# Kernel optimization log

Measured on AMD Instinct MI355X. Metric: run time of the kernel, lower is better.

## Reference

```python
import jax, jax.numpy as jnp
import numpy as np

N_HEAD = 16
N_KV = 4
HEAD_DIM = 128
EPS = 1e-6


def setup_inputs() -> dict:
    key = jax.random.key(0)
    k1, k2, k3 = jax.random.split(key, 3)
    d_model = N_HEAD * HEAD_DIM
    qkv_out = (N_HEAD + 2 * N_KV) * HEAD_DIM
    B, T = 2, 2048
    x = jax.random.normal(k1, (B, T, d_model), dtype=jnp.float32)
    W_qkv = jax.random.normal(k2, (d_model, qkv_out), dtype=jnp.float32) * (d_model ** -0.5)
    W_proj = jax.random.normal(k3, (d_model, d_model), dtype=jnp.float32) * (d_model ** -0.5)
    q_scale = jnp.ones((HEAD_DIM,), dtype=jnp.float32)
    k_scale = jnp.ones((HEAD_DIM,), dtype=jnp.float32)
    return {"x": x, "W_qkv": W_qkv, "W_proj": W_proj, "q_scale": q_scale, "k_scale": k_scale}


def _rms_norm(t):
    return t * jax.lax.rsqrt(jnp.mean(t * t, axis=-1, keepdims=True) + EPS)


def reference(x, W_qkv, W_proj, q_scale, k_scale):
    B, T, C = x.shape
    qkv = x @ W_qkv  # [B, T, (H+2*KV)*D]
    q, k, v = jnp.split(qkv, [N_HEAD * HEAD_DIM, (N_HEAD + N_KV) * HEAD_DIM], axis=-1)
    q = q.reshape(B, T, N_HEAD, HEAD_DIM).transpose(0, 2, 1, 3)  # [B,H,T,D]
    k = k.reshape(B, T, N_KV, HEAD_DIM).transpose(0, 2, 1, 3)    # [B,KV,T,D]
    v = v.reshape(B, T, N_KV, HEAD_DIM).transpose(0, 2, 1, 3)
    # QK RMS-norm with learned per-dim scales
    q = _rms_norm(q) * q_scale
    k = _rms_norm(k) * k_scale
    # GQA: repeat kv heads to match query heads
    rep = N_HEAD // N_KV
    k = jnp.repeat(k, rep, axis=1)
    v = jnp.repeat(v, rep, axis=1)
    # causal SDPA
    scale = 1.0 / jnp.sqrt(jnp.float32(HEAD_DIM))
    scores = jnp.einsum('bhqd,bhkd->bhqk', q, k) * scale
    causal = jnp.tril(jnp.ones((T, T), dtype=bool))
    scores = jnp.where(causal, scores, jnp.finfo(scores.dtype).min)
    attn = jax.nn.softmax(scores, axis=-1)
    y = jnp.einsum('bhqk,bhkd->bhqd', attn, v)  # [B,H,T,D]
    y = y.transpose(0, 2, 1, 3).reshape(B, T, C)
    return y @ W_proj
```

## Files before the change

kernel.cpp:

```cpp
#include <hip/hip_runtime.h>

typedef __bf16 bf16;
typedef __bf16 bf16x8 __attribute__((ext_vector_type(8)));
typedef __bf16 bf16x4 __attribute__((ext_vector_type(4)));
typedef float f32x4 __attribute__((ext_vector_type(4)));
typedef float f32x16 __attribute__((ext_vector_type(16)));
typedef unsigned u32x4 __attribute__((ext_vector_type(4)));

#define EXP2F(x) __builtin_amdgcn_exp2f(x)

#define LOAD_LDS16(gp, lp)                                                     \
  __builtin_amdgcn_global_load_lds(                                            \
      (const __attribute__((address_space(1))) void*)(gp),                     \
      (__attribute__((address_space(3))) void*)(lp), 16, 0, 0)

__global__ __launch_bounds__(256) void k_cvt_x(const float* __restrict__ in,
                                               bf16* __restrict__ out, int n4) {
  int i = blockIdx.x * 256 + threadIdx.x;
  if (i < n4) {
    float4 v = ((const float4*)in)[i];
    bf16x4 o = {(bf16)v.x, (bf16)v.y, (bf16)v.z, (bf16)v.w};
    ((bf16x4*)out)[i] = o;
  }
}

__global__ __launch_bounds__(256) void k_transpose(const float* __restrict__ in,
                                                   bf16* __restrict__ out,
                                                   int R, int C) {
  __shared__ bf16 t[64 * 65];
  int tid = threadIdx.x;
  int c0 = blockIdx.x * 64, r0 = blockIdx.y * 64;
#pragma unroll
  for (int i = 0; i < 16; ++i) {
    int f = i * 256 + tid;
    int rl = f >> 6, cl = f & 63;
    t[rl * 65 + cl] = (bf16)in[(size_t)(r0 + rl) * C + c0 + cl];
  }
  __syncthreads();
#pragma unroll
  for (int i = 0; i < 16; ++i) {
    int f = i * 256 + tid;
    int cl = f >> 6, rl = f & 63;
    out[(size_t)(c0 + cl) * R + r0 + rl] = t[rl * 65 + cl];
  }
}

template <typename OutT, int BM>
__global__ __launch_bounds__(512, 2) void k_gemm256(const bf16* __restrict__ A,
                                                    const bf16* __restrict__ Bt,
                                                    OutT* __restrict__ C,
                                                    int M, int N, int K) {
  constexpr int ASZ = 4 * BM * 8;
  constexpr int MREP = BM / 32;
  __shared__ alignas(16) bf16 As[2][2][ASZ];
  __shared__ alignas(16) bf16 Bs[2][2][4 * 256 * 8];
  int tid = threadIdx.x;
  int wid = tid >> 6, lane = tid & 63;
  int g = lane >> 4, lr = lane & 15;
  int wrow = (wid >> 2) * (BM / 2), wcol = (wid & 3) * 64;
  int gx = gridDim.x;
  int flat = blockIdx.y * gx + blockIdx.x;
  int cpx = (gx * gridDim.y) >> 3;
  int f2 = (flat & 7) * cpx + (flat >> 3);
  int row0 = (f2 % gx) * BM, col0 = (f2 / gx) * 256;
  int NT = K >> 6;
  f32x4 acc[MREP][4] = {};

  auto stageA = [&](int buf, int kh, int kt) {
#pragma unroll
    for (int pass = 0; pass < BM / 128; ++pass) {
      int slot = pass * 512 + tid;
      int kseg, row;
      if constexpr (BM == 256) { kseg = slot >> 8; row = slot & 255; }
      else { kseg = slot >> 7; row = slot & 127; }
      LOAD_LDS16(A + (size_t)(row0 + row) * K + kt * 64 + kh * 32 + kseg * 8,
                 &As[buf][kh][slot * 8]);
    }
  };
  auto stageB = [&](int buf, int kh, int kt) {
#pragma unroll
    for (int pass = 0; pass < 2; ++pass) {
      int slot = pass * 512 + tid;
      int kseg = slot >> 8, row = slot & 255;
      LOAD_LDS16(Bt + (size_t)(col0 + row) * K + kt * 64 + kh * 32 + kseg * 8,
                 &Bs[buf][kh][slot * 8]);
    }
  };
  auto dsA = [&](int buf, int s, int mq, bf16x8* af) {
#pragma unroll
    for (int i = 0; i < 4; ++i)
      af[i] = *(const bf16x8*)&As[buf][s]
                  [(g * BM + wrow + (mq * 4 + i) * 16 + lr) * 8];
  };
  auto dsB = [&](int buf, int s, bf16x8* bfr) {
#pragma unroll
    for (int i = 0; i < 4; ++i)
      bfr[i] = *(const bf16x8*)&Bs[buf][s][((g << 8) + wcol + i * 16 + lr) * 8];
  };
  auto mfma16 = [&](int mq, bf16x8* af, bf16x8* bfr) {
    __builtin_amdgcn_s_setprio(1);
#pragma unroll
    for (int i = 0; i < 4; ++i)
#pragma unroll
      for (int n = 0; n < 4; ++n)
        acc[mq * 4 + i][n] = __builtin_amdgcn_mfma_f32_16x16x32_bf16(
            af[i], bfr[n], acc[mq * 4 + i][n], 0, 0, 0);
    __builtin_amdgcn_s_setprio(0);
  };

  stageA(0, 0, 0);
  stageB(0, 0, 0);
  stageA(0, 1, 0);
  stageB(0, 1, 0);
  if constexpr (BM == 256)
    asm volatile("s_waitcnt vmcnt(4)" ::: "memory");
  else
    asm volatile("s_waitcnt vmcnt(3)" ::: "memory");
  __builtin_amdgcn_s_barrier();

  for (int T = 0; T < NT; ++T) {
    int buf = T & 1, nbuf = buf ^ 1;
    bool more = (T + 1 < NT);
    bf16x8 af[4], bfr[4];
    if constexpr (BM == 256) {
      dsA(buf, 0, 0, af);
      dsB(buf, 0, bfr);
      if (more) stageA(nbuf, 0, T + 1);
      __builtin_amdgcn_s_barrier();
      mfma16(0, af, bfr);
      __builtin_amdgcn_s_barrier();
      dsA(buf, 0, 1, af);
      if (more) {
        stageB(nbuf, 0, T + 1);
        asm volatile("s_waitcnt vmcnt(4)" ::: "memory");
      } else {
        asm volatile("s_waitcnt vmcnt(0)" ::: "memory");
      }
      __builtin_amdgcn_s_barrier();
      mfma16(1, af, bfr);
      __builtin_amdgcn_s_barrier();
      dsA(buf, 1, 0, af);
      dsB(buf, 1, bfr);
      if (more) stageA(nbuf, 1, T + 1);
      __builtin_amdgcn_s_barrier();
      mfma16(0, af, bfr);
      __builtin_amdgcn_s_barrier();
      dsA(buf, 1, 1, af);
      if (more) {
        stageB(nbuf, 1, T + 1);
        asm volatile("s_waitcnt vmcnt(4)" ::: "memory");
      }
      __builtin_amdgcn_s_barrier();
      mfma16(1, af, bfr);
      __builtin_amdgcn_s_barrier();
    } else {
      dsA(buf, 0, 0, af);
      dsB(buf, 0, bfr);
      if (more) {
        stageA(nbuf, 0, T + 1);
        stageB(nbuf, 0, T + 1);
        asm volatile("s_waitcnt vmcnt(3)" ::: "memory");
      } else {
        asm volatile("s_waitcnt vmcnt(0)" ::: "memory");
      }
      __builtin_amdgcn_s_barrier();
      mfma16(0, af, bfr);
      __builtin_amdgcn_s_barrier();
      dsA(buf, 1, 0, af);
      dsB(buf, 1, bfr);
      if (more) {
        stageA(nbuf, 1, T + 1);
        stageB(nbuf, 1, T + 1);
        asm volatile("s_waitcnt vmcnt(3)" ::: "memory");
      }
      __builtin_amdgcn_s_barrier();
      mfma16(0, af, bfr);
      __builtin_amdgcn_s_barrier();
    }
  }

#pragma unroll
  for (int mi = 0; mi < MREP; ++mi)
#pragma unroll
    for (int ni = 0; ni < 4; ++ni) {
      int rb = row0 + wrow + mi * 16 + g * 4;
      int cc = col0 + wcol + ni * 16 + lr;
#pragma unroll
      for (int r = 0; r < 4; ++r) {
        float v = acc[mi][ni][r];
        C[(size_t)(rb + r) * N + cc] = (OutT)v;
      }
    }
}

__global__ __launch_bounds__(256) void k_qknorm(bf16* __restrict__ qkv,
                                                const float* __restrict__ qs,
                                                const float* __restrict__ ks) {
  int tok = blockIdx.x;
  int wid = threadIdx.x >> 6, lane = threadIdx.x & 63;
  int d = lane * 2;
  bf16* rowp = qkv + (size_t)tok * 3072;
#pragma unroll
  for (int i = 0; i < 5; ++i) {
    int cb = (i < 4) ? (wid + i * 4) * 128 : 2048 + wid * 128;
    float v0 = (float)rowp[cb + d], v1 = (float)rowp[cb + d + 1];
    float ss = v0 * v0 + v1 * v1;
#pragma unroll
    for (int off = 1; off < 64; off <<= 1) ss += __shfl_xor(ss, off);
    float r = rsqrtf(ss * (1.0f / 128.0f) + 1e-6f);
    float s0, s1, extra;
    if (i < 4) {
      s0 = qs[d]; s1 = qs[d + 1];
      extra = 0.08838834764831845f * 1.4426950408889634f;
    } else {
      s0 = ks[d]; s1 = ks[d + 1]; extra = 1.0f;
    }
    rowp[cb + d] = (bf16)(v0 * r * s0 * extra);
    rowp[cb + d + 1] = (bf16)(v1 * r * s1 * extra);
  }
}

__global__ __launch_bounds__(256) void k_vt(const bf16* __restrict__ qkv,
                                            bf16* __restrict__ Vt) {
  __shared__ bf16 t[64 * 65];
  int tid = threadIdx.x;
  int t0 = blockIdx.x * 64, d0 = blockIdx.y * 64;
  int bh = blockIdx.z;
  int b = bh >> 2, kvh = bh & 3;
  const bf16* src = qkv + (size_t)(b * 2048) * 3072 + 2560 + kvh * 128;
  bf16* dst = Vt + (size_t)bh * 128 * 2048;
#pragma unroll
  for (int i = 0; i < 16; ++i) {
    int f = i * 256 + tid;
    int tl = f >> 6, dl = f & 63;
    t[tl * 65 + dl] = src[(size_t)(t0 + tl) * 3072 + d0 + dl];
  }
  __syncthreads();
#pragma unroll
  for (int i = 0; i < 16; ++i) {
    int f = i * 256 + tid;
    int dl = f >> 6, tl = f & 63;
    dst[(size_t)(d0 + dl) * 2048 + t0 + tl] = t[tl * 65 + dl];
  }
}

__device__ inline unsigned pack2bf(float a, float b) {
  union { bf16 h[2]; unsigned u; } x;
  x.h[0] = (bf16)a;
  x.h[1] = (bf16)b;
  return x.u;
}

__global__ __launch_bounds__(256, 2) void k_attn(const bf16* __restrict__ qkv,
                                                 const bf16* __restrict__ Vt,
                                                 bf16* __restrict__ y) {
  int flat = blockIdx.x;
  int xcd = flat & 7, iw = flat >> 3;
  int h = xcd + 8 * (iw & 1);
  int rem = iw >> 1;
  int b = rem >> 4;
  int qt = 15 - (rem & 15);
  int kvh = h >> 2;
  int tid = threadIdx.x;
  int wid = tid >> 6, lane = tid & 63;
  int qc = lane & 31, hi = lane >> 5;
  __shared__ alignas(16) bf16 Ks[2][16 * 64 * 8];
  __shared__ alignas(16) bf16 Vs[2][128 * 64];
  const bf16* Qb = qkv + (size_t)(b * 2048) * 3072 + h * 128;
  const bf16* Kb = qkv + (size_t)(b * 2048) * 3072 + 2048 + kvh * 128;
  const bf16* Vb = Vt + (size_t)(b * 4 + kvh) * 128 * 2048;
  int qw0 = qt * 128 + wid * 32;
  int qg = qw0 + qc;
  bf16x8 qf[8];
#pragma unroll
  for (int s = 0; s < 8; ++s)
    qf[s] = *(const bf16x8*)&Qb[(size_t)qg * 3072 + s * 16 + hi * 8];
  f32x16 acc[4] = {};
  float mrun = -1e30f, lrun = 0.f;

  auto STAGE = [&](int buf, int kt2) {
    int s0 = kt2 * 64;
#pragma unroll
    for (int i = 0; i < 4; ++i) {
      int slot = i * 256 + tid;
      int ch = slot >> 6, row = slot & 63;
      LOAD_LDS16(Kb + (size_t)(s0 + row) * 3072 + ch * 8, &Ks[buf][slot * 8]);
    }
#pragma unroll
    for (int i = 0; i < 4; ++i) {
      int slot = i * 256 + tid;
      int d = slot >> 3, c = slot & 7;
      LOAD_LDS16(Vb + (size_t)d * 2048 + s0 + ((c ^ (d & 7)) * 8),
                 &Vs[buf][slot * 8]);
    }
  };

  STAGE(0, 0);
  int cur = 0;
  int ktmax = 2 * qt + 1;
  for (int kt = 0; kt <= ktmax; ++kt) {
    int s0 = kt * 64;
    if (kt < ktmax) {
      STAGE(cur ^ 1, kt + 1);
      asm volatile("s_waitcnt vmcnt(8)" ::: "memory");
    } else {
      asm volatile("s_waitcnt vmcnt(0)" ::: "memory");
    }
    __builtin_amdgcn_s_barrier();
    __builtin_amdgcn_sched_barrier(0);
    if (s0 <= qw0 + 31) {
      f32x16 sc[2] = {};
#pragma unroll
      for (int s = 0; s < 8; ++s)
#pragma unroll
        for (int n = 0; n < 2; ++n) {
          bf16x8 kf =
              *(const bf16x8*)&Ks[cur][(((2 * s + hi) << 6) + n * 32 + qc) * 8];
          sc[n] =
              __builtin_amdgcn_mfma_f32_32x32x16_bf16(kf, qf[s], sc[n], 0, 0, 0);
        }
      if (s0 + 63 > qw0) {
#pragma unroll
        for (int n = 0; n < 2; ++n)
#pragma unroll
          for (int r = 0; r < 16; ++r) {
            int kg = s0 + n * 32 + (r & 3) + 8 * (r >> 2) + 4 * hi;
            if (kg > qg) sc[n][r] = -1e30f;
          }
      }
      float pm = -1e30f;
#pragma unroll
      for (int n = 0; n < 2; ++n)
#pragma unroll
        for (int r = 0; r < 16; ++r) pm = fmaxf(pm, sc[n][r]);
      pm = fmaxf(pm, __shfl_xor(pm, 32));
      if (__any(pm > mrun + 11.0f)) {
        float mnew = fmaxf(mrun, pm);
        float scl = EXP2F(mrun - mnew);
        mrun = mnew;
        lrun *= scl;
        float sv[16];
#pragma unroll
        for (int r = 0; r < 16; ++r)
          sv[r] = __shfl(scl, (r & 3) + 8 * (r >> 2) + 4 * hi);
#pragma unroll
        for (int dt = 0; dt < 4; ++dt)
#pragma unroll
          for (int r = 0; r < 16; ++r) acc[dt][r] *= sv[r];
      }
      float rs = 0.f;
#pragma unroll
      for (int n = 0; n < 2; ++n) {
        unsigned pk[8];
#pragma unroll
        for (int mm = 0; mm < 8; ++mm) {
          float e0 = EXP2F(sc[n][2 * mm] - mrun);
          float e1 = EXP2F(sc[n][2 * mm + 1] - mrun);
          rs += e0 + e1;
          pk[mm] = pack2bf(e0, e1);
        }
#pragma unroll
        for (int l2 = 0; l2 < 2; ++l2) {
          unsigned a0 = pk[4 * l2 + 0], b0 = pk[4 * l2 + 2];
          unsigned a1 = pk[4 * l2 + 1], b1 = pk[4 * l2 + 3];
          asm volatile("v_permlane32_swap_b32 %0, %1" : "+v"(a0), "+v"(b0));
          asm volatile("v_permlane32_swap_b32 %0, %1" : "+v"(a1), "+v"(b1));
          u32x4 w = {a0, a1, b0, b1};
          bf16x8 pf = __builtin_bit_cast(bf16x8, w);
          int ksg = 2 * n + l2;
#pragma unroll
          for (int dt = 0; dt < 4; ++dt) {
            int drow = dt * 32 + qc;
            bf16x8 vf = *(const bf16x8*)&Vs[cur][(drow * 8 +
                                                  ((2 * ksg + hi) ^ (qc & 7))) *
                                                 8];
            acc[dt] =
                __builtin_amdgcn_mfma_f32_32x32x16_bf16(pf, vf, acc[dt], 0, 0, 0);
          }
        }
      }
      rs += __shfl_xor(rs, 32);
      lrun += rs;
    }
    __builtin_amdgcn_s_barrier();
    cur ^= 1;
  }
  float rlv = 1.0f / lrun;
  float rcl[16];
#pragma unroll
  for (int r = 0; r < 16; ++r)
    rcl[r] = __shfl(rlv, (r & 3) + 8 * (r >> 2) + 4 * hi);
#pragma unroll
  for (int dt = 0; dt < 4; ++dt)
#pragma unroll
    for (int r = 0; r < 16; ++r) {
      int row = qw0 + (r & 3) + 8 * (r >> 2) + 4 * hi;
      float v = acc[dt][r] * rcl[r];
      y[(size_t)(b * 2048 + row) * 2048 + h * 128 + dt * 32 + qc] = (bf16)v;
    }
}

extern "C" void kernel_launch(void* const* d_in, const int* in_sizes, int n_in,
                              void* d_out, int out_size, void* d_ws,
                              size_t ws_size, hipStream_t stream) {
  const float* x = (const float*)d_in[0];
  const float* Wqkv = (const float*)d_in[1];
  const float* Wproj = (const float*)d_in[2];
  const float* qs = (const float*)d_in[3];
  const float* ks = (const float*)d_in[4];
  float* out = (float*)d_out;
  char* ws = (char*)d_ws;

  bf16* xb = (bf16*)(ws);
  bf16* Wqkvt = (bf16*)(ws + (size_t)(16u << 20));
  bf16* Wprojt = (bf16*)(ws + (size_t)(28u << 20));
  bf16* qkv = (bf16*)(ws + (size_t)(36u << 20));
  bf16* Vt = Wqkvt;
  bf16* y = xb;

  k_cvt_x<<<8192, 256, 0, stream>>>(x, xb, 8388608 / 4);
  k_transpose<<<dim3(3072 / 64, 2048 / 64), 256, 0, stream>>>(Wqkv, Wqkvt, 2048, 3072);
  k_transpose<<<dim3(2048 / 64, 2048 / 64), 256, 0, stream>>>(Wproj, Wprojt, 2048, 2048);
  k_gemm256<bf16, 256><<<dim3(16, 12), 512, 0, stream>>>(xb, Wqkvt, qkv, 4096, 3072, 2048);
  k_qknorm<<<4096, 256, 0, stream>>>(qkv, qs, ks);
  k_vt<<<dim3(32, 2, 8), 256, 0, stream>>>(qkv, Vt);
  k_attn<<<dim3(512, 1, 1), 256, 0, stream>>>(qkv, Vt, y);
  k_gemm256<float, 128><<<dim3(32, 8), 512, 0, stream>>>(y, Wprojt, out, 4096, 2048, 2048);
}
```

Baseline: 259.4 us.

## Use 128x128 GEMM for QKV projection and pre-tile V for contiguous attention loads

Adds a 128x128-tile, 256-thread GEMM kernel and uses it for the QKV projection, giving 768 workgroups in place of 192 for better CU occupancy. The V transpose now writes V in a chunked [tile][kchunk][d][8] layout so attention staging can load each 64-key tile as one contiguous block. The XOR-swizzled LDS reads for V are replaced with direct indexing, and a sched_barrier is added before the loop-end barrier. The risk is that the unswizzled V LDS reads cause bank conflicts, and the simpler GEMM pipeline waits on vmcnt(0) every iteration.

Result: slower. 290.5 us (+12.0%).

```diff
diff --git a/kernel.cpp b/kernel.cpp
--- a/kernel.cpp
+++ b/kernel.cpp
@@ -43,6 +43,85 @@
     int cl = f >> 6, rl = f & 63;
     out[(size_t)(c0 + cl) * R + r0 + rl] = t[rl * 65 + cl];
   }
+}
+
+template <typename OutT>
+__global__ __launch_bounds__(256, 3) void k_gemm128(const bf16* __restrict__ A,
+                                                    const bf16* __restrict__ Bt,
+                                                    OutT* __restrict__ C,
+                                                    int M, int N, int K) {
+  __shared__ alignas(16) bf16 As[2][4 * 128 * 8];
+  __shared__ alignas(16) bf16 Bs[2][4 * 128 * 8];
+  int tid = threadIdx.x;
+  int wid = tid >> 6, lane = tid & 63;
+  int g = lane >> 4, lr = lane & 15;
+  int wrow = (wid >> 1) * 64, wcol = (wid & 1) * 64;
+  int gx = gridDim.x;
+  int flat = blockIdx.y * gx + blockIdx.x;
+  int cpx = (gx * gridDim.y) >> 3;
+  int f2 = (flat & 7) * cpx + (flat >> 3);
+  int row0 = (f2 % gx) * 128, col0 = (f2 / gx) * 128;
+  int NT = K >> 5;
+  f32x4 acc[4][4] = {};
+
+  auto stageA = [&](int buf, int kt) {
+#pragma unroll
+    for (int pass = 0; pass < 2; ++pass) {
+      int slot = pass * 256 + tid;
+      int kseg = slot >> 7, row = slot & 127;
+      LOAD_LDS16(A + (size_t)(row0 + row) * K + kt * 32 + kseg * 8,
+                 &As[buf][slot * 8]);
+    }
+  };
+  auto stageB = [&](int buf, int kt) {
+#pragma unroll
+    for (int pass = 0; pass < 2; ++pass) {
+      int slot = pass * 256 + tid;
+      int kseg = slot >> 7, row = slot & 127;
+      LOAD_LDS16(Bt + (size_t)(col0 + row) * K + kt * 32 + kseg * 8,
+                 &Bs[buf][slot * 8]);
+    }
+  };
+
+  stageA(0, 0);
+  stageB(0, 0);
+  asm volatile("s_waitcnt vmcnt(0)" ::: "memory");
+  __builtin_amdgcn_s_barrier();
+
+  for (int T = 0; T < NT; ++T) {
+    int buf = T & 1;
+    if (T + 1 < NT) {
+      stageA(buf ^ 1, T + 1);
+      stageB(buf ^ 1, T + 1);
+    }
+    bf16x8 af[4], bfr[4];
+#pragma unroll
+    for (int i = 0; i < 4; ++i)
+      af[i] = *(const bf16x8*)&As[buf][((g << 7) + wrow + i * 16 + lr) * 8];
+#pragma unroll
+    for (int i = 0; i < 4; ++i)
+      bfr[i] = *(const bf16x8*)&Bs[buf][((g << 7) + wcol + i * 16 + lr) * 8];
+    __builtin_amdgcn_s_setprio(1);
+#pragma unroll
+    for (int i = 0; i < 4; ++i)
+#pragma unroll
+      for (int n = 0; n < 4; ++n)
+        acc[i][n] = __builtin_amdgcn_mfma_f32_16x16x32_bf16(af[i], bfr[n],
+                                                            acc[i][n], 0, 0, 0);
+    __builtin_amdgcn_s_setprio(0);
+    asm volatile("s_waitcnt vmcnt(0)" ::: "memory");
+    __builtin_amdgcn_s_barrier();
+  }
+
+#pragma unroll
+  for (int mi = 0; mi < 4; ++mi)
+#pragma unroll
+    for (int ni = 0; ni < 4; ++ni) {
+      int rb = row0 + wrow + mi * 16 + g * 4;
+      int cc = col0 + wcol + ni * 16 + lr;
+#pragma unroll
+      for (int r = 0; r < 4; ++r) C[(size_t)(rb + r) * N + cc] = (OutT)acc[mi][ni][r];
+    }
 }
 
 template <typename OutT, int BM>
@@ -186,10 +265,7 @@
       int rb = row0 + wrow + mi * 16 + g * 4;
       int cc = col0 + wcol + ni * 16 + lr;
 #pragma unroll
-      for (int r = 0; r < 4; ++r) {
-        float v = acc[mi][ni][r];
-        C[(size_t)(rb + r) * N + cc] = (OutT)v;
-      }
+      for (int r = 0; r < 4; ++r) C[(size_t)(rb + r) * N + cc] = (OutT)acc[mi][ni][r];
     }
 }
 
@@ -228,7 +304,7 @@
   int bh = blockIdx.z;
   int b = bh >> 2, kvh = bh & 3;
   const bf16* src = qkv + (size_t)(b * 2048) * 3072 + 2560 + kvh * 128;
-  bf16* dst = Vt + (size_t)bh * 128 * 2048;
+  bf16* dst = Vt + (size_t)bh * 262144 + (size_t)(t0 >> 6) * 8192;
 #pragma unroll
   for (int i = 0; i < 16; ++i) {
     int f = i * 256 + tid;
@@ -237,10 +313,13 @@
   }
   __syncthreads();
 #pragma unroll
-  for (int i = 0; i < 16; ++i) {
-    int f = i * 256 + tid;
-    int dl = f >> 6, tl = f & 63;
-    dst[(size_t)(d0 + dl) * 2048 + t0 + tl] = t[tl * 65 + dl];
+  for (int i = 0; i < 2; ++i) {
+    int v = i * 256 + tid;
+    int c = v >> 6, dv = v & 63;
+    bf16x8 o;
+#pragma unroll
+    for (int j = 0; j < 8; ++j) o[j] = t[(c * 8 + j) * 65 + dv];
+    *(bf16x8*)&dst[(size_t)c * 1024 + (size_t)(d0 + dv) * 8] = o;
   }
 }
 
@@ -265,10 +344,10 @@
   int wid = tid >> 6, lane = tid & 63;
   int qc = lane & 31, hi = lane >> 5;
   __shared__ alignas(16) bf16 Ks[2][16 * 64 * 8];
-  __shared__ alignas(16) bf16 Vs[2][128 * 64];
+  __shared__ alignas(16) bf16 Vs[2][8 * 128 * 8];
   const bf16* Qb = qkv + (size_t)(b * 2048) * 3072 + h * 128;
   const bf16* Kb = qkv + (size_t)(b * 2048) * 3072 + 2048 + kvh * 128;
-  const bf16* Vb = Vt + (size_t)(b * 4 + kvh) * 128 * 2048;
+  const bf16* Vb = Vt + (size_t)(b * 4 + kvh) * 262144;
   int qw0 = qt * 128 + wid * 32;
   int qg = qw0 + qc;
   bf16x8 qf[8];
@@ -289,9 +368,7 @@
 #pragma unroll
     for (int i = 0; i < 4; ++i) {
       int slot = i * 256 + tid;
-      int d = slot >> 3, c = slot & 7;
-      LOAD_LDS16(Vb + (size_t)d * 2048 + s0 + ((c ^ (d & 7)) * 8),
-                 &Vs[buf][slot * 8]);
+      LOAD_LDS16(Vb + (size_t)kt2 * 8192 + slot * 8, &Vs[buf][slot * 8]);
     }
   };
 
@@ -367,13 +444,11 @@
           asm volatile("v_permlane32_swap_b32 %0, %1" : "+v"(a1), "+v"(b1));
           u32x4 w = {a0, a1, b0, b1};
           bf16x8 pf = __builtin_bit_cast(bf16x8, w);
-          int ksg = 2 * n + l2;
+          int c = 2 * (2 * n + l2) + hi;
 #pragma unroll
           for (int dt = 0; dt < 4; ++dt) {
-            int drow = dt * 32 + qc;
-            bf16x8 vf = *(const bf16x8*)&Vs[cur][(drow * 8 +
-                                                  ((2 * ksg + hi) ^ (qc & 7))) *
-                                                 8];
+            bf16x8 vf =
+                *(const bf16x8*)&Vs[cur][((c << 7) + dt * 32 + qc) * 8];
             acc[dt] =
                 __builtin_amdgcn_mfma_f32_32x32x16_bf16(pf, vf, acc[dt], 0, 0, 0);
           }
@@ -382,6 +457,7 @@
       rs += __shfl_xor(rs, 32);
       lrun += rs;
     }
+    __builtin_amdgcn_sched_barrier(0);
     __builtin_amdgcn_s_barrier();
     cur ^= 1;
   }
@@ -421,7 +497,7 @@
   k_cvt_x<<<8192, 256, 0, stream>>>(x, xb, 8388608 / 4);
   k_transpose<<<dim3(3072 / 64, 2048 / 64), 256, 0, stream>>>(Wqkv, Wqkvt, 2048, 3072);
   k_transpose<<<dim3(2048 / 64, 2048 / 64), 256, 0, stream>>>(Wproj, Wprojt, 2048, 2048);
-  k_gemm256<bf16, 256><<<dim3(16, 12), 512, 0, stream>>>(xb, Wqkvt, qkv, 4096, 3072, 2048);
+  k_gemm128<bf16><<<dim3(32, 24), 256, 0, stream>>>(xb, Wqkvt, qkv, 4096, 3072, 2048);
   k_qknorm<<<4096, 256, 0, stream>>>(qkv, qs, ks);
   k_vt<<<dim3(32, 2, 8), 256, 0, stream>>>(qkv, Vt);
   k_attn<<<dim3(512, 1, 1), 256, 0, stream>>>(qkv, Vt, y);
```

## Tile V transpose into contiguous per-block chunks and reorder attention block schedule

Applied to the files above, without the earlier changes.

The V transpose kernel now writes V in a tiled layout: each 64-token block is a contiguous 8192-element chunk of [chunk][d][8]. Its stores become vectorized 16-byte writes, and the attention kernel stages each V tile with fully linear loads instead of XOR-swizzled strided ones. The attention grid mapping now pairs heavy and light causal query tiles across two launch slots, and batch is interleaved, to balance per-CU work. An extra sched_barrier is added before the trailing barrier. The new V LDS layout drops the swizzle, which risks bank conflicts on the PV fragment reads.

New measurement: 250.9 us. -3.3%, faster.

```diff
diff --git a/kernel.cpp b/kernel.cpp
--- a/kernel.cpp
+++ b/kernel.cpp
@@ -186,10 +186,7 @@
       int rb = row0 + wrow + mi * 16 + g * 4;
       int cc = col0 + wcol + ni * 16 + lr;
 #pragma unroll
-      for (int r = 0; r < 4; ++r) {
-        float v = acc[mi][ni][r];
-        C[(size_t)(rb + r) * N + cc] = (OutT)v;
-      }
+      for (int r = 0; r < 4; ++r) C[(size_t)(rb + r) * N + cc] = (OutT)acc[mi][ni][r];
     }
 }
 
@@ -228,7 +225,7 @@
   int bh = blockIdx.z;
   int b = bh >> 2, kvh = bh & 3;
   const bf16* src = qkv + (size_t)(b * 2048) * 3072 + 2560 + kvh * 128;
-  bf16* dst = Vt + (size_t)bh * 128 * 2048;
+  bf16* dst = Vt + (size_t)bh * 262144 + (size_t)(t0 >> 6) * 8192;
 #pragma unroll
   for (int i = 0; i < 16; ++i) {
     int f = i * 256 + tid;
@@ -237,10 +234,13 @@
   }
   __syncthreads();
 #pragma unroll
-  for (int i = 0; i < 16; ++i) {
-    int f = i * 256 + tid;
-    int dl = f >> 6, tl = f & 63;
-    dst[(size_t)(d0 + dl) * 2048 + t0 + tl] = t[tl * 65 + dl];
+  for (int i = 0; i < 2; ++i) {
+    int v = i * 256 + tid;
+    int c = v >> 6, dv = v & 63;
+    bf16x8 o;
+#pragma unroll
+    for (int j = 0; j < 8; ++j) o[j] = t[(c * 8 + j) * 65 + dv];
+    *(bf16x8*)&dst[(size_t)c * 1024 + (size_t)(d0 + dv) * 8] = o;
   }
 }
 
@@ -255,20 +255,22 @@
                                                  const bf16* __restrict__ Vt,
                                                  bf16* __restrict__ y) {
   int flat = blockIdx.x;
-  int xcd = flat & 7, iw = flat >> 3;
+  int slot = flat >> 8;
+  int j = flat & 255;
+  int xcd = j & 7, iw = j >> 3;
   int h = xcd + 8 * (iw & 1);
-  int rem = iw >> 1;
-  int b = rem >> 4;
-  int qt = 15 - (rem & 15);
+  int r = iw >> 1;
+  int b = r & 1;
+  int qt = slot ? (r >> 1) : (15 - (r >> 1));
   int kvh = h >> 2;
   int tid = threadIdx.x;
   int wid = tid >> 6, lane = tid & 63;
   int qc = lane & 31, hi = lane >> 5;
   __shared__ alignas(16) bf16 Ks[2][16 * 64 * 8];
-  __shared__ alignas(16) bf16 Vs[2][128 * 64];
+  __shared__ alignas(16) bf16 Vs[2][8 * 128 * 8];
   const bf16* Qb = qkv + (size_t)(b * 2048) * 3072 + h * 128;
   const bf16* Kb = qkv + (size_t)(b * 2048) * 3072 + 2048 + kvh * 128;
-  const bf16* Vb = Vt + (size_t)(b * 4 + kvh) * 128 * 2048;
+  const bf16* Vb = Vt + (size_t)(b * 4 + kvh) * 262144;
   int qw0 = qt * 128 + wid * 32;
   int qg = qw0 + qc;
   bf16x8 qf[8];
@@ -282,16 +284,14 @@
     int s0 = kt2 * 64;
 #pragma unroll
     for (int i = 0; i < 4; ++i) {
-      int slot = i * 256 + tid;
-      int ch = slot >> 6, row = slot & 63;
-      LOAD_LDS16(Kb + (size_t)(s0 + row) * 3072 + ch * 8, &Ks[buf][slot * 8]);
+      int sl = i * 256 + tid;
+      int ch = sl >> 6, row = sl & 63;
+      LOAD_LDS16(Kb + (size_t)(s0 + row) * 3072 + ch * 8, &Ks[buf][sl * 8]);
     }
 #pragma unroll
     for (int i = 0; i < 4; ++i) {
-      int slot = i * 256 + tid;
-      int d = slot >> 3, c = slot & 7;
-      LOAD_LDS16(Vb + (size_t)d * 2048 + s0 + ((c ^ (d & 7)) * 8),
-                 &Vs[buf][slot * 8]);
+      int sl = i * 256 + tid;
+      LOAD_LDS16(Vb + (size_t)kt2 * 8192 + sl * 8, &Vs[buf][sl * 8]);
     }
   };
 
@@ -323,16 +323,16 @@
 #pragma unroll
         for (int n = 0; n < 2; ++n)
 #pragma unroll
-          for (int r = 0; r < 16; ++r) {
-            int kg = s0 + n * 32 + (r & 3) + 8 * (r >> 2) + 4 * hi;
-            if (kg > qg) sc[n][r] = -1e30f;
+          for (int r2 = 0; r2 < 16; ++r2) {
+            int kg = s0 + n * 32 + (r2 & 3) + 8 * (r2 >> 2) + 4 * hi;
+            if (kg > qg) sc[n][r2] = -1e30f;
           }
       }
       float pm = -1e30f;
 #pragma unroll
       for (int n = 0; n < 2; ++n)
 #pragma unroll
-        for (int r = 0; r < 16; ++r) pm = fmaxf(pm, sc[n][r]);
+        for (int r2 = 0; r2 < 16; ++r2) pm = fmaxf(pm, sc[n][r2]);
       pm = fmaxf(pm, __shfl_xor(pm, 32));
       if (__any(pm > mrun + 11.0f)) {
         float mnew = fmaxf(mrun, pm);
@@ -341,12 +341,12 @@
         lrun *= scl;
         float sv[16];
 #pragma unroll
-        for (int r = 0; r < 16; ++r)
-          sv[r] = __shfl(scl, (r & 3) + 8 * (r >> 2) + 4 * hi);
+        for (int r2 = 0; r2 < 16; ++r2)
+          sv[r2] = __shfl(scl, (r2 & 3) + 8 * (r2 >> 2) + 4 * hi);
 #pragma unroll
         for (int dt = 0; dt < 4; ++dt)
 #pragma unroll
-          for (int r = 0; r < 16; ++r) acc[dt][r] *= sv[r];
+          for (int r2 = 0; r2 < 16; ++r2) acc[dt][r2] *= sv[r2];
       }
       float rs = 0.f;
 #pragma unroll
@@ -367,13 +367,11 @@
           asm volatile("v_permlane32_swap_b32 %0, %1" : "+v"(a1), "+v"(b1));
           u32x4 w = {a0, a1, b0, b1};
           bf16x8 pf = __builtin_bit_cast(bf16x8, w);
-          int ksg = 2 * n + l2;
+          int c = 2 * (2 * n + l2) + hi;
 #pragma unroll
           for (int dt = 0; dt < 4; ++dt) {
-            int drow = dt * 32 + qc;
-            bf16x8 vf = *(const bf16x8*)&Vs[cur][(drow * 8 +
-                                                  ((2 * ksg + hi) ^ (qc & 7))) *
-                                                 8];
+            bf16x8 vf =
+                *(const bf16x8*)&Vs[cur][((c << 7) + dt * 32 + qc) * 8];
             acc[dt] =
                 __builtin_amdgcn_mfma_f32_32x32x16_bf16(pf, vf, acc[dt], 0, 0, 0);
           }
@@ -382,20 +380,21 @@
       rs += __shfl_xor(rs, 32);
       lrun += rs;
     }
+    __builtin_amdgcn_sched_barrier(0);
     __builtin_amdgcn_s_barrier();
     cur ^= 1;
   }
   float rlv = 1.0f / lrun;
   float rcl[16];
 #pragma unroll
-  for (int r = 0; r < 16; ++r)
-    rcl[r] = __shfl(rlv, (r & 3) + 8 * (r >> 2) + 4 * hi);
+  for (int r2 = 0; r2 < 16; ++r2)
+    rcl[r2] = __shfl(rlv, (r2 & 3) + 8 * (r2 >> 2) + 4 * hi);
 #pragma unroll
   for (int dt = 0; dt < 4; ++dt)
 #pragma unroll
-    for (int r = 0; r < 16; ++r) {
-      int row = qw0 + (r & 3) + 8 * (r >> 2) + 4 * hi;
-      float v = acc[dt][r] * rcl[r];
+    for (int r2 = 0; r2 < 16; ++r2) {
+      int row = qw0 + (r2 & 3) + 8 * (r2 >> 2) + 4 * hi;
+      float v = acc[dt][r2] * rcl[r2];
       y[(size_t)(b * 2048 + row) * 2048 + h * 128 + dt * 32 + qc] = (bf16)v;
     }
 }
```
